# Optimization experiments

Measured on AMD Instinct MI355X. Metric: run time of the kernel, lower is better.

Reference implementation:

```python
import jax, jax.numpy as jnp
import numpy as np

GROUP_SIZE = 128


def _unpack_int4(packed):
    # packed: [..., P] int32, each holding 8 int4 nibbles (LSB-first).
    u = jax.lax.bitcast_convert_type(packed, jnp.uint32)
    shifts = jnp.arange(8, dtype=jnp.uint32) * 4  # nibble bit offsets
    vals = (u[..., None] >> shifts) & jnp.uint32(15)  # [..., P, 8]
    return vals.reshape(*packed.shape[:-1], -1)  # [..., P*8] in [0, 15]


def setup_inputs() -> dict:
    key = jax.random.key(0)
    k1, k2, k3, k4 = jax.random.split(key, 4)
    B, S, K, O = 4, 16, 4096, 11008
    G = K // GROUP_SIZE          # 32 groups
    GP = (G + 7) // 8            # 4 packed-zero columns
    imax = np.iinfo(np.int32).max
    x = jax.random.normal(k1, (B, S, K), dtype=jnp.float16)
    qweight_i32 = jax.random.randint(k2, (O, K // 8), 0, imax, dtype=jnp.int32)
    qzeros_i32 = jax.random.randint(k3, (O, GP), 0, imax, dtype=jnp.int32)
    scales_f16 = jax.random.uniform(k4, (O, G), dtype=jnp.float16,
                                    minval=0.001, maxval=0.02)
    return {"x": x, "qweight_i32": qweight_i32, "qzeros_i32": qzeros_i32,
            "scales_f16": scales_f16}


def reference(x, qweight_i32, qzeros_i32, scales_f16):
    O, G = scales_f16.shape
    K = G * GROUP_SIZE
    # Dequantize: w = (q - z) * s, per-group int4 quantization.
    q = _unpack_int4(qweight_i32)[:, :K].astype(jnp.float16)       # [O, K]
    z = _unpack_int4(qzeros_i32)[:, :G].astype(jnp.float16)        # [O, G]
    z_k = jnp.repeat(z, GROUP_SIZE, axis=1)                        # [O, K]
    s_k = jnp.repeat(scales_f16, GROUP_SIZE, axis=1)               # [O, K]
    w = (q - z_k) * s_k                                            # fp16 [O, K]
    x2d = x.reshape(-1, K).astype(jnp.float16)                     # [m, K]
    out = jnp.matmul(x2d, w.T).astype(jnp.float32)                 # [m, O]
    return out.reshape(*x.shape[:-1], O)
```

## Files before the change

### kernel.cpp

```cpp
#include <hip/hip_runtime.h>
#include <stdint.h>

typedef _Float16 half8  __attribute__((ext_vector_type(8)));
typedef float    floatx4 __attribute__((ext_vector_type(4)));
typedef uint32_t uint4v  __attribute__((ext_vector_type(4)));

#define KDIM   4096
#define ODIM   11008
#define NG     32
#define K8     512
#define KU     512
#define KSPLIT 8
#define GPB    4
#define OBLK   172
#define PART_ELEMS (64 * ODIM)
#define LDS_PITCH 20

__device__ __forceinline__ uint32_t pk_f16(float a, float b) {
    return __builtin_bit_cast(uint32_t, __builtin_amdgcn_cvt_pkrtz(a, b));
}

__global__ __launch_bounds__(256) void cvt_x_kernel(
    const float4* __restrict__ x, uint4v* __restrict__ xh,
    float* __restrict__ xsumT)
{
    const size_t i = (size_t)blockIdx.x * 256 + threadIdx.x;
    const float4 f0 = x[2 * i];
    const float4 f1 = x[2 * i + 1];
    xh[i] = uint4v{pk_f16(f0.x, f1.x), pk_f16(f0.y, f1.y),
                   pk_f16(f0.z, f1.z), pk_f16(f0.w, f1.w)};

    float p = f0.x + f0.y + f0.z + f0.w + f1.x + f1.y + f1.z + f1.w;
    p += __shfl_xor(p, 1);
    p += __shfl_xor(p, 2);
    p += __shfl_xor(p, 4);
    p += __shfl_xor(p, 8);
    if ((threadIdx.x & 15) == 0) {
        const size_t k0 = i * 8;
        const int m = (int)(k0 >> 12);
        const int g = (int)(k0 >> 7) & 31;
        xsumT[g * 64 + m] = p;
    }
}

__global__ __launch_bounds__(256) void reduce_kernel(
    const float4* __restrict__ part, float4* __restrict__ out)
{
    const size_t i = (size_t)blockIdx.x * 256 + threadIdx.x;
    float4 a = part[i];
    #pragma unroll
    for (int kb = 1; kb < KSPLIT; ++kb) {
        const float4 b = part[(size_t)kb * (PART_ELEMS / 4) + i];
        a.x += b.x; a.y += b.y; a.z += b.z; a.w += b.w;
    }
    out[i] = a;
}

__global__ __launch_bounds__(256, 4) void w4a16_kernel(
    const uint4v*   __restrict__ xh,
    const uint32_t* __restrict__ qw,
    const uint32_t* __restrict__ qz,
    const float*    __restrict__ sc,
    const float*    __restrict__ xsumT,
    float*          __restrict__ part)
{
    __shared__ uint32_t qlds[2][64 * LDS_PITCH];

    const int t    = threadIdx.x;
    const int wv   = t >> 6;
    const int lane = t & 63;
    const int q    = lane >> 4;
    const int ml   = lane & 15;

    const int ob = blockIdx.x % OBLK;
    const int kb = blockIdx.x / OBLK;
    const int o0 = ob * 64;
    const int g0 = kb * GPB;

    const int srow = wv * 16 + (lane >> 2);
    const int schk = lane & 3;
    const uint32_t* sgp = qw + (size_t)(o0 + srow) * K8 + g0 * 16 + schk * 4;
    const int widx = srow * LDS_PITCH + schk * 4;

    const uint4v* xp = xh + (size_t)(wv * 16 + ml) * KU + (size_t)g0 * 16 + q * 4;

    uint32_t zdw[4];
    floatx4  svec[4];
    #pragma unroll
    for (int sub = 0; sub < 4; ++sub) {
        const int o = o0 + sub * 16 + ml;
        zdw[sub]  = qz[(size_t)o * 4 + (g0 >> 3)];
        svec[sub] = *reinterpret_cast<const floatx4*>(sc + (size_t)o * NG + g0);
    }
    const int zsh0 = (g0 & 7) * 4;

    const int mrow = wv * 16 + q * 4;
    floatx4 xsv[GPB];
    #pragma unroll
    for (int g = 0; g < GPB; ++g)
        xsv[g] = *reinterpret_cast<const floatx4*>(xsumT + (g0 + g) * 64 + mrow);

    floatx4 acc[4] = {{0.f,0.f,0.f,0.f},{0.f,0.f,0.f,0.f},
                      {0.f,0.f,0.f,0.f},{0.f,0.f,0.f,0.f}};

    uint4v sv = *reinterpret_cast<const uint4v*>(sgp);

    #pragma unroll
    for (int g = 0; g < GPB; ++g) {
        *reinterpret_cast<uint4v*>(&qlds[g & 1][widx]) = sv;
        __syncthreads();
        if (g + 1 < GPB)
            sv = *reinterpret_cast<const uint4v*>(sgp + (g + 1) * 16);

        uint4v ax[4];
        #pragma unroll
        for (int ks = 0; ks < 4; ++ks)
            ax[ks] = xp[g * 16 + ks];

        uint4v qf[4];
        #pragma unroll
        for (int sub = 0; sub < 4; ++sub)
            qf[sub] = *reinterpret_cast<const uint4v*>(
                &qlds[g & 1][(sub * 16 + ml) * LDS_PITCH + q * 4]);

        #pragma unroll
        for (int sub = 0; sub < 4; ++sub) {
            const uint32_t zn  = (zdw[sub] >> (zsh0 + g * 4)) & 0xFu;
            const float    s   = svec[sub][g];
            const float    czs = s * (1024.0f + (float)zn);

            floatx4 tmp = {0.f, 0.f, 0.f, 0.f};
            #pragma unroll
            for (int ks = 0; ks < 4; ++ks) {
                const uint32_t ud = qf[sub][ks];
                const uint4v bw = {
                    ( ud         & 0x000F000Fu) | 0x64006400u,
                    ((ud >> 4)   & 0x000F000Fu) | 0x64006400u,
                    ((ud >> 8)   & 0x000F000Fu) | 0x64006400u,
                    ((ud >> 12)  & 0x000F000Fu) | 0x64006400u};
                const half8 b = __builtin_bit_cast(half8, bw);
                tmp = __builtin_amdgcn_mfma_f32_16x16x32_f16(
                    __builtin_bit_cast(half8, ax[ks]), b, tmp, 0, 0, 0);
            }
            #pragma unroll
            for (int r = 0; r < 4; ++r)
                acc[sub][r] += s * tmp[r] - czs * xsv[g][r];
        }
    }

    float* pb = part + (size_t)kb * PART_ELEMS;
    #pragma unroll
    for (int sub = 0; sub < 4; ++sub) {
        float* op = pb + (size_t)mrow * ODIM + (o0 + sub * 16 + ml);
        op[0]                  = acc[sub][0];
        op[(size_t)ODIM]       = acc[sub][1];
        op[2 * (size_t)ODIM]   = acc[sub][2];
        op[3 * (size_t)ODIM]   = acc[sub][3];
    }
}

extern "C" void kernel_launch(void* const* d_in, const int* in_sizes, int n_in,
                              void* d_out, int out_size, void* d_ws, size_t ws_size,
                              hipStream_t stream) {
    const float*    x       = (const float*)d_in[0];
    const uint32_t* qweight = (const uint32_t*)d_in[1];
    const uint32_t* qzeros  = (const uint32_t*)d_in[2];
    const float*    scales  = (const float*)d_in[3];
    float* out = (float*)d_out;

    uint4v* xh    = (uint4v*)d_ws;
    float*  xsumT = (float*)((char*)d_ws + 512 * 1024);
    float*  part  = (float*)((char*)d_ws + 1024 * 1024);

    cvt_x_kernel<<<dim3(128), dim3(256), 0, stream>>>((const float4*)x, xh, xsumT);
    w4a16_kernel<<<dim3(OBLK * KSPLIT), dim3(256), 0, stream>>>(
        xh, qweight, qzeros, scales, xsumT, part);
    reduce_kernel<<<dim3(688), dim3(256), 0, stream>>>(
        (const float4*)part, (float4*)out);
}
```

Baseline: 100.2 us.

## Halve K-split, pre-swizzle fp16 activations, double-buffer activation loads

Reduces the K-split from 8 to 4 so each block covers 8 groups. This halves the partial-sum traffic written by the GEMM and read back by the reduce pass. The converted activations are stored in a fragment-major layout so each lane's MFMA operand load is coalesced, and the next group's activations are prefetched into a register double buffer. Launch bounds drop to 2 blocks per CU and the reduce kernel becomes grid-strided with fewer blocks. The costs are fewer GEMM blocks (688 instead of 1376), which may underfill the device, and higher register use.

```diff
diff --git a/kernel.cpp b/kernel.cpp
--- a/kernel.cpp
+++ b/kernel.cpp
@@ -8,63 +8,63 @@
 #define KDIM   4096
 #define ODIM   11008
 #define NG     32
-#define K8     512
-#define KU     512
-#define KSPLIT 8
-#define GPB    4
+#define KSPLIT 4
+#define GPB    8
 #define OBLK   172
+#define PITCH  20
 #define PART_ELEMS (64 * ODIM)
-#define LDS_PITCH 20
 
 __device__ __forceinline__ uint32_t pk_f16(float a, float b) {
     return __builtin_bit_cast(uint32_t, __builtin_amdgcn_cvt_pkrtz(a, b));
 }
 
 __global__ __launch_bounds__(256) void cvt_x_kernel(
-    const float4* __restrict__ x, uint4v* __restrict__ xh,
+    const float4* __restrict__ x, uint4v* __restrict__ xh2,
     float* __restrict__ xsumT)
 {
-    const size_t i = (size_t)blockIdx.x * 256 + threadIdx.x;
+    const int i = blockIdx.x * 256 + threadIdx.x;
     const float4 f0 = x[2 * i];
     const float4 f1 = x[2 * i + 1];
-    xh[i] = uint4v{pk_f16(f0.x, f1.x), pk_f16(f0.y, f1.y),
-                   pk_f16(f0.z, f1.z), pk_f16(f0.w, f1.w)};
+    const uint4v v = {pk_f16(f0.x, f1.x), pk_f16(f0.y, f1.y),
+                      pk_f16(f0.z, f1.z), pk_f16(f0.w, f1.w)};
+    const int m  = i >> 9, c = i & 511;
+    const int g  = c >> 4, cg = c & 15, q = cg >> 2, ks = cg & 3;
+    const int mt = m >> 4, ml = m & 15;
+    xh2[((size_t)(g * 4 + ks) * 4 + mt) * 64 + q * 16 + ml] = v;
 
     float p = f0.x + f0.y + f0.z + f0.w + f1.x + f1.y + f1.z + f1.w;
     p += __shfl_xor(p, 1);
     p += __shfl_xor(p, 2);
     p += __shfl_xor(p, 4);
     p += __shfl_xor(p, 8);
-    if ((threadIdx.x & 15) == 0) {
-        const size_t k0 = i * 8;
-        const int m = (int)(k0 >> 12);
-        const int g = (int)(k0 >> 7) & 31;
-        xsumT[g * 64 + m] = p;
-    }
+    if ((threadIdx.x & 15) == 0) xsumT[g * 64 + m] = p;
 }
 
 __global__ __launch_bounds__(256) void reduce_kernel(
     const float4* __restrict__ part, float4* __restrict__ out)
 {
-    const size_t i = (size_t)blockIdx.x * 256 + threadIdx.x;
-    float4 a = part[i];
-    #pragma unroll
-    for (int kb = 1; kb < KSPLIT; ++kb) {
-        const float4 b = part[(size_t)kb * (PART_ELEMS / 4) + i];
-        a.x += b.x; a.y += b.y; a.z += b.z; a.w += b.w;
+    const int NT = OBLK * 256;
+    for (int i = blockIdx.x * 256 + threadIdx.x;
+         i < PART_ELEMS / 4; i += NT) {
+        float4 a = part[i];
+        #pragma unroll
+        for (int kb = 1; kb < KSPLIT; ++kb) {
+            const float4 b = part[(size_t)kb * (PART_ELEMS / 4) + i];
+            a.x += b.x; a.y += b.y; a.z += b.z; a.w += b.w;
+        }
+        out[i] = a;
     }
-    out[i] = a;
 }
 
-__global__ __launch_bounds__(256, 4) void w4a16_kernel(
-    const uint4v*   __restrict__ xh,
+__global__ __launch_bounds__(256, 2) void w4a16_kernel(
+    const uint4v*   __restrict__ xh2,
     const uint32_t* __restrict__ qw,
     const uint32_t* __restrict__ qz,
     const float*    __restrict__ sc,
     const float*    __restrict__ xsumT,
     float*          __restrict__ part)
 {
-    __shared__ uint32_t qlds[2][64 * LDS_PITCH];
+    __shared__ uint32_t qlds[2][64 * PITCH];
 
     const int t    = threadIdx.x;
     const int wv   = t >> 6;
@@ -77,56 +77,61 @@
     const int o0 = ob * 64;
     const int g0 = kb * GPB;
 
-    const int srow = wv * 16 + (lane >> 2);
-    const int schk = lane & 3;
-    const uint32_t* sgp = qw + (size_t)(o0 + srow) * K8 + g0 * 16 + schk * 4;
-    const int widx = srow * LDS_PITCH + schk * 4;
+    const int srow = t >> 2;
+    const int schk = t & 3;
+    const uint32_t* sgp = qw + (size_t)(o0 + srow) * 512 + g0 * 16 + schk * 4;
+    const int widx = srow * PITCH + schk * 4;
 
-    const uint4v* xp = xh + (size_t)(wv * 16 + ml) * KU + (size_t)g0 * 16 + q * 4;
+    const uint4v* xp = xh2 + (size_t)(g0 * 16 + wv) * 64 + lane;
 
     uint32_t zdw[4];
-    floatx4  svec[4];
+    floatx4  svec[4][2];
     #pragma unroll
     for (int sub = 0; sub < 4; ++sub) {
         const int o = o0 + sub * 16 + ml;
-        zdw[sub]  = qz[(size_t)o * 4 + (g0 >> 3)];
-        svec[sub] = *reinterpret_cast<const floatx4*>(sc + (size_t)o * NG + g0);
+        zdw[sub]     = qz[(size_t)o * 4 + kb];
+        svec[sub][0] = *reinterpret_cast<const floatx4*>(sc + (size_t)o * NG + g0);
+        svec[sub][1] = *reinterpret_cast<const floatx4*>(sc + (size_t)o * NG + g0 + 4);
     }
-    const int zsh0 = (g0 & 7) * 4;
 
     const int mrow = wv * 16 + q * 4;
-    floatx4 xsv[GPB];
-    #pragma unroll
-    for (int g = 0; g < GPB; ++g)
-        xsv[g] = *reinterpret_cast<const floatx4*>(xsumT + (g0 + g) * 64 + mrow);
-
     floatx4 acc[4] = {{0.f,0.f,0.f,0.f},{0.f,0.f,0.f,0.f},
                       {0.f,0.f,0.f,0.f},{0.f,0.f,0.f,0.f}};
 
     uint4v sv = *reinterpret_cast<const uint4v*>(sgp);
+    uint4v ax[2][4];
+    #pragma unroll
+    for (int ks = 0; ks < 4; ++ks) ax[0][ks] = xp[ks * 256];
 
     #pragma unroll
     for (int g = 0; g < GPB; ++g) {
         *reinterpret_cast<uint4v*>(&qlds[g & 1][widx]) = sv;
         __syncthreads();
-        if (g + 1 < GPB)
+        if (g + 1 < GPB) {
             sv = *reinterpret_cast<const uint4v*>(sgp + (g + 1) * 16);
+            #pragma unroll
+            for (int ks = 0; ks < 4; ++ks)
+                ax[(g + 1) & 1][ks] = xp[(size_t)(g + 1) * 1024 + ks * 256];
+        }
 
-        uint4v ax[4];
+        half8 afrag[4];
         #pragma unroll
         for (int ks = 0; ks < 4; ++ks)
-            ax[ks] = xp[g * 16 + ks];
+            afrag[ks] = __builtin_bit_cast(half8, ax[g & 1][ks]);
 
         uint4v qf[4];
         #pragma unroll
         for (int sub = 0; sub < 4; ++sub)
             qf[sub] = *reinterpret_cast<const uint4v*>(
-                &qlds[g & 1][(sub * 16 + ml) * LDS_PITCH + q * 4]);
+                &qlds[g & 1][(sub * 16 + ml) * PITCH + q * 4]);
+
+        const floatx4 xsg = *reinterpret_cast<const floatx4*>(
+            xsumT + (g0 + g) * 64 + mrow);
 
         #pragma unroll
         for (int sub = 0; sub < 4; ++sub) {
-            const uint32_t zn  = (zdw[sub] >> (zsh0 + g * 4)) & 0xFu;
-            const float    s   = svec[sub][g];
+            const uint32_t zn  = (zdw[sub] >> (g * 4)) & 0xFu;
+            const float    s   = svec[sub][g >> 2][g & 3];
             const float    czs = s * (1024.0f + (float)zn);
 
             floatx4 tmp = {0.f, 0.f, 0.f, 0.f};
@@ -139,23 +144,22 @@
                     ((ud >> 8)   & 0x000F000Fu) | 0x64006400u,
                     ((ud >> 12)  & 0x000F000Fu) | 0x64006400u};
                 const half8 b = __builtin_bit_cast(half8, bw);
-                tmp = __builtin_amdgcn_mfma_f32_16x16x32_f16(
-                    __builtin_bit_cast(half8, ax[ks]), b, tmp, 0, 0, 0);
+                tmp = __builtin_amdgcn_mfma_f32_16x16x32_f16(afrag[ks], b, tmp, 0, 0, 0);
             }
             #pragma unroll
             for (int r = 0; r < 4; ++r)
-                acc[sub][r] += s * tmp[r] - czs * xsv[g][r];
+                acc[sub][r] += s * tmp[r] - czs * xsg[r];
         }
     }
 
-    float* pb = part + (size_t)kb * PART_ELEMS;
+    float* pb = part + (size_t)kb * PART_ELEMS + (size_t)mrow * ODIM;
     #pragma unroll
     for (int sub = 0; sub < 4; ++sub) {
-        float* op = pb + (size_t)mrow * ODIM + (o0 + sub * 16 + ml);
-        op[0]                  = acc[sub][0];
-        op[(size_t)ODIM]       = acc[sub][1];
-        op[2 * (size_t)ODIM]   = acc[sub][2];
-        op[3 * (size_t)ODIM]   = acc[sub][3];
+        float* op = pb + o0 + sub * 16 + ml;
+        op[0]                = acc[sub][0];
+        op[(size_t)ODIM]     = acc[sub][1];
+        op[2 * (size_t)ODIM] = acc[sub][2];
+        op[3 * (size_t)ODIM] = acc[sub][3];
     }
 }
 
@@ -168,13 +172,13 @@
     const float*    scales  = (const float*)d_in[3];
     float* out = (float*)d_out;
 
-    uint4v* xh    = (uint4v*)d_ws;
+    uint4v* xh2   = (uint4v*)d_ws;
     float*  xsumT = (float*)((char*)d_ws + 512 * 1024);
     float*  part  = (float*)((char*)d_ws + 1024 * 1024);
 
-    cvt_x_kernel<<<dim3(128), dim3(256), 0, stream>>>((const float4*)x, xh, xsumT);
+    cvt_x_kernel<<<dim3(128), dim3(256), 0, stream>>>((const float4*)x, xh2, xsumT);
     w4a16_kernel<<<dim3(OBLK * KSPLIT), dim3(256), 0, stream>>>(
-        xh, qweight, qzeros, scales, xsumT, part);
-    reduce_kernel<<<dim3(688), dim3(256), 0, stream>>>(
+        xh2, qweight, qzeros, scales, xsumT, part);
+    reduce_kernel<<<dim3(OBLK), dim3(256), 0, stream>>>(
         (const float4*)part, (float4*)out);
 }
```

Result: faster. 97.81 us (-2.4%).
